# Kernel optimization log

Hardware: AMD Instinct MI355X
Metric: run time of the kernel (lower is better)

The kernel has to match this reference:

```python
import jax, jax.numpy as jnp
import numpy as np

NUM_HEADS = 8
KERNEL = 7
LOW_RANK = 4


def setup_inputs() -> dict:
    key = jax.random.key(0)
    ks = jax.random.split(key, 10)
    B, H, W, C = 4, 56, 56, 256
    nh, K, lr = NUM_HEADS, KERNEL, LOW_RANK
    s = 0.02
    return {
        "x": jax.random.normal(ks[0], (B, H, W, C), jnp.float32),
        "Wq": jax.random.normal(ks[1], (C, nh * lr), jnp.float32) * s,
        "bq": jnp.zeros((nh * lr,), jnp.float32),
        "Wk": jax.random.normal(ks[2], (C, nh * lr), jnp.float32) * s,
        "bk": jnp.zeros((nh * lr,), jnp.float32),
        "Wv": jax.random.normal(ks[3], (C, C), jnp.float32) * s,
        "bv": jnp.zeros((C,), jnp.float32),
        "rpb": jax.random.normal(ks[4], (nh, 2 * K - 1, 2 * K - 1), jnp.float32) * s,
        "Wp": jax.random.normal(ks[5], (C, C), jnp.float32) * s,
        "bp": jnp.zeros((C,), jnp.float32),
    }


def reference(x, Wq, bq, Wk, bk, Wv, bv, rpb, Wp, bp):
    B, H, W, C = x.shape
    nh, K, lr = NUM_HEADS, KERNEL, LOW_RANK
    hd = C // nh
    r = K // 2
    scale = hd ** -0.5

    # Projections. Note: the original uses a raw reshape (B,H,W,nh*lr)->(B,nh,H,W,lr),
    # which we replicate exactly (row-major reshape, no permute).
    q = (x @ Wq + bq).reshape(B, nh, H, W, lr) * scale
    k = (x @ Wk + bk).reshape(B, nh, H, W, lr)
    v = (x @ Wv + bv).reshape(B, nh, H, W, hd)

    # NATTEN window start indices (clamped so each query sees exactly K keys per axis).
    start_h = jnp.clip(jnp.arange(H) - r, 0, H - K)  # (H,)
    start_w = jnp.clip(jnp.arange(W) - r, 0, W - K)  # (W,)
    idx_h = start_h[:, None] + jnp.arange(K)[None, :]  # (H, K)
    idx_w = start_w[:, None] + jnp.arange(K)[None, :]  # (W, K)

    # Gather local K/V windows: (B, nh, H, K, W, K, d)
    k_win = k[:, :, idx_h][:, :, :, :, idx_w]
    v_win = v[:, :, idx_h][:, :, :, :, idx_w]

    # Scores: (B, nh, H, W, K, K)
    attn = jnp.einsum('bhijc,bhikjlc->bhijkl', q, k_win)

    # Relative position bias indices: (key_pos - query_pos) + (K-1)
    bi = idx_h - jnp.arange(H)[:, None] + (K - 1)  # (H, K)
    bj = idx_w - jnp.arange(W)[:, None] + (K - 1)  # (W, K)
    bias = rpb[:, bi][:, :, :, bj]                 # (nh, H, K, W, K)
    attn = attn + bias.transpose(0, 1, 3, 2, 4)[None]  # (B, nh, H, W, K, K)

    attn = jax.nn.softmax(attn.reshape(B, nh, H, W, K * K), axis=-1)
    attn = attn.reshape(B, nh, H, W, K, K)

    # Weighted aggregation of V windows: (B, nh, H, W, hd)
    out = jnp.einsum('bhijkl,bhikjld->bhijd', attn, v_win)
    out = out.transpose(0, 2, 3, 1, 4).reshape(B, H, W, C)
    return out @ Wp + bp
```

## Files before the change

### kernel.cpp

```cpp
#include <hip/hip_runtime.h>
#include <hip/hip_bf16.h>

#define BD 4
#define HD_ 56
#define WD 56
#define CD 256
#define NH 8
#define KW 7
#define LR 4
#define HDIM 32
#define MB (HD_*WD)
#define NROWS (BD*MB)
#define QK_PER_B (HD_*WD*32)
#define V_PER_B  (HD_*WD*256)

typedef short short8 __attribute__((ext_vector_type(8)));
typedef float floatx4 __attribute__((ext_vector_type(4)));

static __device__ inline ushort f2bf(float f) {
    __hip_bfloat16 h = __float2bfloat16(f);
    return *(ushort*)&h;
}
static __device__ inline float bf2f(uint h16) {
    union { uint u; float f; } c; c.u = h16 << 16; return c.f;
}
static __device__ inline float bf2f_hi(uint u) {
    union { uint v; float f; } c; c.v = u & 0xffff0000u; return c.f;
}

__global__ __launch_bounds__(256) void prep_w(
    const float* __restrict__ Wq, const float* __restrict__ Wk,
    const float* __restrict__ Wv, const float* __restrict__ bq,
    const float* __restrict__ bk, const float* __restrict__ bv,
    const float* __restrict__ Wp,
    ushort* __restrict__ WpkT, ushort* __restrict__ WpT, float* __restrict__ pb)
{
    int idx = blockIdx.x * 256 + threadIdx.x;
    if (idx < 81920) {
        int n = idx >> 8, k = idx & 255;
        float v;
        if (n < 32)       v = Wq[k * 32 + n];
        else if (n < 64)  v = Wk[k * 32 + (n - 32)];
        else              v = Wv[k * 256 + (n - 64)];
        WpkT[idx] = f2bf(v);
    } else if (idx < 81920 + 65536) {
        int j = idx - 81920;
        int n = j >> 8, k = j & 255;
        WpT[j] = f2bf(Wp[k * 256 + n]);
    } else if (idx < 81920 + 65536 + 320) {
        int n = idx - (81920 + 65536);
        pb[n] = (n < 32) ? bq[n] : (n < 64) ? bk[n - 32] : bv[n - 64];
    }
}

__global__ __launch_bounds__(256) void mfma_qkv(
    const float* __restrict__ X, const ushort* __restrict__ Bt,
    const float* __restrict__ pb, ushort* __restrict__ Qb,
    ushort* __restrict__ Kb, ushort* __restrict__ Vb)
{
    __shared__ ushort As[128 * 40];
    __shared__ ushort Bs[64 * 40];

    const int t = threadIdx.x;
    const int m0 = blockIdx.y * 128;
    const int n0 = blockIdx.x * 64;
    const int ar = t >> 1;
    const int ac = (t & 1) << 4;
    const int br = t >> 2;
    const int bc = (t & 3) << 3;
    const int lane = t & 63, w = t >> 6;
    const int col = lane & 15, quad = lane >> 4;
    const int q8 = quad << 3;

    floatx4 acc[2][4] = {};

    for (int k0 = 0; k0 < 256; k0 += 32) {
        float4 a0 = *(const float4*)&X[(m0 + ar) * 256 + k0 + ac];
        float4 a1 = *(const float4*)&X[(m0 + ar) * 256 + k0 + ac + 4];
        float4 a2 = *(const float4*)&X[(m0 + ar) * 256 + k0 + ac + 8];
        float4 a3 = *(const float4*)&X[(m0 + ar) * 256 + k0 + ac + 12];
        uint4 bv = *(const uint4*)&Bt[(n0 + br) * 256 + k0 + bc];
        union { ushort h[8]; uint4 u; } p0, p1;
        p0.h[0] = f2bf(a0.x); p0.h[1] = f2bf(a0.y); p0.h[2] = f2bf(a0.z); p0.h[3] = f2bf(a0.w);
        p0.h[4] = f2bf(a1.x); p0.h[5] = f2bf(a1.y); p0.h[6] = f2bf(a1.z); p0.h[7] = f2bf(a1.w);
        p1.h[0] = f2bf(a2.x); p1.h[1] = f2bf(a2.y); p1.h[2] = f2bf(a2.z); p1.h[3] = f2bf(a2.w);
        p1.h[4] = f2bf(a3.x); p1.h[5] = f2bf(a3.y); p1.h[6] = f2bf(a3.z); p1.h[7] = f2bf(a3.w);
        __syncthreads();
        *(uint4*)&As[ar * 40 + ac]     = p0.u;
        *(uint4*)&As[ar * 40 + ac + 8] = p1.u;
        *(uint4*)&Bs[br * 40 + bc]     = bv;
        __syncthreads();
#pragma unroll
        for (int s = 0; s < 2; ++s) {
            short8 af = *(short8*)&As[((w << 5) + (s << 4) + col) * 40 + q8];
#pragma unroll
            for (int nt = 0; nt < 4; ++nt) {
                short8 bf = *(short8*)&Bs[((nt << 4) + col) * 40 + q8];
                acc[s][nt] = __builtin_amdgcn_mfma_f32_16x16x32_bf16(af, bf, acc[s][nt], 0, 0, 0);
            }
        }
    }

#pragma unroll
    for (int s = 0; s < 2; ++s) {
#pragma unroll
        for (int nt = 0; nt < 4; ++nt) {
            int gn = n0 + (nt << 4) + col;
            float bias = pb[gn];
#pragma unroll
            for (int rg = 0; rg < 4; ++rg) {
                int m = m0 + (w << 5) + (s << 4) + (quad << 2) + rg;
                ushort h = f2bf(acc[s][nt][rg] + bias);
                if (n0 == 0 && nt < 2)      Qb[m * 32 + gn] = h;
                else if (n0 == 0)           Kb[m * 32 + (gn - 32)] = h;
                else                        Vb[m * 256 + (gn - 64)] = h;
            }
        }
    }
}

__global__ __launch_bounds__(256) void mfma_out(
    const ushort* __restrict__ Ag, const ushort* __restrict__ Bt,
    const float* __restrict__ bp, float* __restrict__ out)
{
    __shared__ ushort As[128 * 40];
    __shared__ ushort Bs[64 * 40];

    const int t = threadIdx.x;
    const int m0 = blockIdx.y * 128;
    const int n0 = blockIdx.x * 64;
    const int ar = t >> 1;
    const int ac = (t & 1) << 4;
    const int br = t >> 2;
    const int bc = (t & 3) << 3;
    const int lane = t & 63, w = t >> 6;
    const int col = lane & 15, quad = lane >> 4;
    const int q8 = quad << 3;

    floatx4 acc[2][4] = {};

    for (int k0 = 0; k0 < 256; k0 += 32) {
        uint4 av0 = *(const uint4*)&Ag[(m0 + ar) * 256 + k0 + ac];
        uint4 av1 = *(const uint4*)&Ag[(m0 + ar) * 256 + k0 + ac + 8];
        uint4 bv  = *(const uint4*)&Bt[(n0 + br) * 256 + k0 + bc];
        __syncthreads();
        *(uint4*)&As[ar * 40 + ac]     = av0;
        *(uint4*)&As[ar * 40 + ac + 8] = av1;
        *(uint4*)&Bs[br * 40 + bc]     = bv;
        __syncthreads();
#pragma unroll
        for (int s = 0; s < 2; ++s) {
            short8 af = *(short8*)&As[((w << 5) + (s << 4) + col) * 40 + q8];
#pragma unroll
            for (int nt = 0; nt < 4; ++nt) {
                short8 bf = *(short8*)&Bs[((nt << 4) + col) * 40 + q8];
                acc[s][nt] = __builtin_amdgcn_mfma_f32_16x16x32_bf16(af, bf, acc[s][nt], 0, 0, 0);
            }
        }
    }

#pragma unroll
    for (int s = 0; s < 2; ++s) {
#pragma unroll
        for (int nt = 0; nt < 4; ++nt) {
            int gn = n0 + (nt << 4) + col;
            float bias = bp[gn];
#pragma unroll
            for (int rg = 0; rg < 4; ++rg) {
                int m = m0 + (w << 5) + (s << 4) + (quad << 2) + rg;
                out[m * 256 + gn] = acc[s][nt][rg] + bias;
            }
        }
    }
}

__global__ __launch_bounds__(256, 8) void natten_attn_t(
    const ushort* __restrict__ Qb, const ushort* __restrict__ Kb,
    const ushort* __restrict__ Vb, const float* __restrict__ rpb,
    ushort* __restrict__ Ab)
{
    __shared__ float4 Ksf[196];
    __shared__ float4 Vsf[8 * 197];
    __shared__ float  Rs[169];

    const int tj = blockIdx.x, ti = blockIdx.y;
    const int n = blockIdx.z & 7, b = blockIdx.z >> 3;
    const int t = threadIdx.x;
    const int i0 = ti * 8, j0 = tj * 8;
    const int rs = min(max(i0 - 3, 0), HD_ - 14);
    const int cs = min(max(j0 - 3, 0), WD - 14);

    const ushort* kb = Kb + b * QK_PER_B + n * (HD_ * WD * LR);
    const ushort* vb = Vb + b * V_PER_B + n * (HD_ * WD * HDIM);

    if (t < 196) {
        int r = t / 14, c = t % 14;
        union { uint2 u; uint w[2]; } kr;
        kr.u = *(const uint2*)&kb[(rs + r) * (WD * LR) + (cs + c) * LR];
        Ksf[t] = make_float4(bf2f(kr.w[0] & 0xffff), bf2f_hi(kr.w[0]),
                             bf2f(kr.w[1] & 0xffff), bf2f_hi(kr.w[1]));
    }
    if (t < 169) Rs[t] = rpb[n * 169 + t];
    for (int idx = t; idx < 784; idx += 256) {
        int oct = idx & 3, pos = idx >> 2;
        int r = pos / 14, c = pos % 14;
        union { uint4 u; uint w[4]; } vr;
        vr.u = *(const uint4*)&vb[(rs + r) * (WD * HDIM) + (cs + c) * HDIM + oct * 8];
        Vsf[(2 * oct) * 197 + pos] =
            make_float4(bf2f(vr.w[0] & 0xffff), bf2f_hi(vr.w[0]),
                        bf2f(vr.w[1] & 0xffff), bf2f_hi(vr.w[1]));
        Vsf[(2 * oct + 1) * 197 + pos] =
            make_float4(bf2f(vr.w[2] & 0xffff), bf2f_hi(vr.w[2]),
                        bf2f(vr.w[3] & 0xffff), bf2f_hi(vr.w[3]));
    }
    __syncthreads();

    const int q  = t >> 2, p = t & 3;
    const int qi = q >> 3, qj = q & 7;
    const int i = i0 + qi, j = j0 + qj;
    const int sh = min(max(i - 3, 0), HD_ - KW);
    const int sw = min(max(j - 3, 0), WD - KW);
    const int oh = sh - rs, ow = sw - cs;

    union { uint2 u; uint w[2]; } qr;
    qr.u = *(const uint2*)&Qb[b * QK_PER_B + n * (HD_ * WD * LR) + i * (WD * LR) + j * LR];
    const float scale = 0.17677669529663687f;
    float qx = bf2f(qr.w[0] & 0xffff) * scale, qy = bf2f_hi(qr.w[0]) * scale;
    float qz = bf2f(qr.w[1] & 0xffff) * scale, qw = bf2f_hi(qr.w[1]) * scale;

    const int rb0 = (sh - i + 6) * 13 + (sw - j + 6);

    float sum = 0.f;
    float a[8] = {0.f, 0.f, 0.f, 0.f, 0.f, 0.f, 0.f, 0.f};
    const float4* v0 = &Vsf[(2 * p) * 197];
    const float4* v1 = &Vsf[(2 * p + 1) * 197];
    for (int kh = 0; kh < KW; ++kh) {
        int kpos  = (oh + kh) * 14 + ow;
        int rbase = rb0 + kh * 13;
#pragma unroll
        for (int kw = 0; kw < KW; ++kw) {
            float4 kf = Ksf[kpos + kw];
            float d = Rs[rbase + kw];
            d = fmaf(qx, kf.x, d);
            d = fmaf(qy, kf.y, d);
            d = fmaf(qz, kf.z, d);
            d = fmaf(qw, kf.w, d);
            float e = __expf(d);
            sum += e;
            float4 x0 = v0[kpos + kw];
            float4 x1 = v1[kpos + kw];
            a[0] = fmaf(e, x0.x, a[0]); a[1] = fmaf(e, x0.y, a[1]);
            a[2] = fmaf(e, x0.z, a[2]); a[3] = fmaf(e, x0.w, a[3]);
            a[4] = fmaf(e, x1.x, a[4]); a[5] = fmaf(e, x1.y, a[5]);
            a[6] = fmaf(e, x1.z, a[6]); a[7] = fmaf(e, x1.w, a[7]);
        }
    }
    float inv = 1.0f / sum;

    union { ushort h[8]; uint4 u; } pk;
#pragma unroll
    for (int c = 0; c < 8; ++c) pk.h[c] = f2bf(a[c] * inv);
    *(uint4*)&Ab[(((b * HD_ + i) * WD + j)) * CD + n * HDIM + p * 8] = pk.u;
}

extern "C" void kernel_launch(void* const* d_in, const int* in_sizes, int n_in,
                              void* d_out, int out_size, void* d_ws, size_t ws_size,
                              hipStream_t stream) {
    const float* x   = (const float*)d_in[0];
    const float* Wq  = (const float*)d_in[1];
    const float* bq  = (const float*)d_in[2];
    const float* Wk  = (const float*)d_in[3];
    const float* bk  = (const float*)d_in[4];
    const float* Wv  = (const float*)d_in[5];
    const float* bv  = (const float*)d_in[6];
    const float* rpb = (const float*)d_in[7];
    const float* Wp  = (const float*)d_in[8];
    const float* bp  = (const float*)d_in[9];
    float* out = (float*)d_out;

    ushort* WpkT = (ushort*)d_ws;
    ushort* WpT  = WpkT + 81920;
    ushort* Ab   = WpT + 65536;
    ushort* Qb   = Ab + 3211264;
    ushort* Kb   = Qb + BD * QK_PER_B;
    ushort* Vb   = Kb + BD * QK_PER_B;
    float*  pb   = (float*)(Vb + BD * V_PER_B);

    prep_w<<<(81920 + 65536 + 320 + 255) / 256, 256, 0, stream>>>(
        Wq, Wk, Wv, bq, bk, bv, Wp, WpkT, WpT, pb);

    mfma_qkv<<<dim3(5, NROWS / 128), 256, 0, stream>>>(x, WpkT, pb, Qb, Kb, Vb);

    natten_attn_t<<<dim3(7, 7, 32), 256, 0, stream>>>(Qb, Kb, Vb, rpb, Ab);

    mfma_out<<<dim3(4, NROWS / 128), 256, 0, stream>>>(Ab, WpT, bp, out);
}
```

Before: 120.4 us.

## Fuse all four stages into one persistent kernel with grid barriers

Replaces the four separate launches (weight prep, QKV GEMM, neighborhood attention, output GEMM) with one persistent kernel of 512 blocks. Each stage loops over its former blocks as jobs, and software grid barriers built on atomics in the workspace separate the stages. The aim is to remove per-launch overhead and the gaps between kernels. In exchange, the grid barriers rely on all 512 blocks being resident at once, occupancy drops to 2 blocks per CU, and the attention stage (1568 jobs) now runs in several waves with no overlap between stages.

```diff
diff --git a/kernel.cpp b/kernel.cpp
--- a/kernel.cpp
+++ b/kernel.cpp
@@ -14,6 +14,9 @@
 #define QK_PER_B (HD_*WD*32)
 #define V_PER_B  (HD_*WD*256)
 
+#define GRID_G 512
+#define MAGICF 0xC0FFEE01u
+
 typedef short short8 __attribute__((ext_vector_type(8)));
 typedef float floatx4 __attribute__((ext_vector_type(4)));
 
@@ -28,239 +31,274 @@
     union { uint v; float f; } c; c.v = u & 0xffff0000u; return c.f;
 }
 
-__global__ __launch_bounds__(256) void prep_w(
+static __device__ inline void grid_barrier(uint* cnt, uint* gen) {
+    __syncthreads();
+    if (threadIdx.x == 0) {
+        __threadfence();
+        uint g = __hip_atomic_load(gen, __ATOMIC_RELAXED, __HIP_MEMORY_SCOPE_AGENT);
+        uint a = __hip_atomic_fetch_add(cnt, 1u, __ATOMIC_ACQ_REL, __HIP_MEMORY_SCOPE_AGENT);
+        if (a == GRID_G - 1) {
+            __hip_atomic_store(cnt, 0u, __ATOMIC_RELAXED, __HIP_MEMORY_SCOPE_AGENT);
+            __hip_atomic_fetch_add(gen, 1u, __ATOMIC_RELEASE, __HIP_MEMORY_SCOPE_AGENT);
+        } else {
+            while (__hip_atomic_load(gen, __ATOMIC_ACQUIRE, __HIP_MEMORY_SCOPE_AGENT) == g)
+                __builtin_amdgcn_s_sleep(1);
+        }
+        __threadfence();
+    }
+    __syncthreads();
+}
+
+__global__ __launch_bounds__(256, 2) void fused_all(
+    const float* __restrict__ X,
     const float* __restrict__ Wq, const float* __restrict__ Wk,
     const float* __restrict__ Wv, const float* __restrict__ bq,
     const float* __restrict__ bk, const float* __restrict__ bv,
-    const float* __restrict__ Wp,
-    ushort* __restrict__ WpkT, ushort* __restrict__ WpT, float* __restrict__ pb)
+    const float* __restrict__ rpb,
+    const float* __restrict__ Wp, const float* __restrict__ bp,
+    ushort* __restrict__ WpkT, ushort* __restrict__ WpT,
+    float* __restrict__ pb,
+    ushort* __restrict__ Qb, ushort* __restrict__ Kb, ushort* __restrict__ Vb,
+    ushort* __restrict__ Ab, float* __restrict__ out,
+    uint* __restrict__ bar)
 {
-    int idx = blockIdx.x * 256 + threadIdx.x;
-    if (idx < 81920) {
-        int n = idx >> 8, k = idx & 255;
-        float v;
-        if (n < 32)       v = Wq[k * 32 + n];
-        else if (n < 64)  v = Wk[k * 32 + (n - 32)];
-        else              v = Wv[k * 256 + (n - 64)];
-        WpkT[idx] = f2bf(v);
-    } else if (idx < 81920 + 65536) {
-        int j = idx - 81920;
-        int n = j >> 8, k = j & 255;
-        WpT[j] = f2bf(Wp[k * 256 + n]);
-    } else if (idx < 81920 + 65536 + 320) {
-        int n = idx - (81920 + 65536);
-        pb[n] = (n < 32) ? bq[n] : (n < 64) ? bk[n - 32] : bv[n - 64];
-    }
-}
-
-__global__ __launch_bounds__(256) void mfma_qkv(
-    const float* __restrict__ X, const ushort* __restrict__ Bt,
-    const float* __restrict__ pb, ushort* __restrict__ Qb,
-    ushort* __restrict__ Kb, ushort* __restrict__ Vb)
-{
-    __shared__ ushort As[128 * 40];
-    __shared__ ushort Bs[64 * 40];
+    __shared__ __align__(16) char smem[29184];
 
     const int t = threadIdx.x;
-    const int m0 = blockIdx.y * 128;
-    const int n0 = blockIdx.x * 64;
-    const int ar = t >> 1;
-    const int ac = (t & 1) << 4;
-    const int br = t >> 2;
-    const int bc = (t & 3) << 3;
-    const int lane = t & 63, w = t >> 6;
-    const int col = lane & 15, quad = lane >> 4;
-    const int q8 = quad << 3;
-
-    floatx4 acc[2][4] = {};
-
-    for (int k0 = 0; k0 < 256; k0 += 32) {
-        float4 a0 = *(const float4*)&X[(m0 + ar) * 256 + k0 + ac];
-        float4 a1 = *(const float4*)&X[(m0 + ar) * 256 + k0 + ac + 4];
-        float4 a2 = *(const float4*)&X[(m0 + ar) * 256 + k0 + ac + 8];
-        float4 a3 = *(const float4*)&X[(m0 + ar) * 256 + k0 + ac + 12];
-        uint4 bv = *(const uint4*)&Bt[(n0 + br) * 256 + k0 + bc];
-        union { ushort h[8]; uint4 u; } p0, p1;
-        p0.h[0] = f2bf(a0.x); p0.h[1] = f2bf(a0.y); p0.h[2] = f2bf(a0.z); p0.h[3] = f2bf(a0.w);
-        p0.h[4] = f2bf(a1.x); p0.h[5] = f2bf(a1.y); p0.h[6] = f2bf(a1.z); p0.h[7] = f2bf(a1.w);
-        p1.h[0] = f2bf(a2.x); p1.h[1] = f2bf(a2.y); p1.h[2] = f2bf(a2.z); p1.h[3] = f2bf(a2.w);
-        p1.h[4] = f2bf(a3.x); p1.h[5] = f2bf(a3.y); p1.h[6] = f2bf(a3.z); p1.h[7] = f2bf(a3.w);
-        __syncthreads();
-        *(uint4*)&As[ar * 40 + ac]     = p0.u;
-        *(uint4*)&As[ar * 40 + ac + 8] = p1.u;
-        *(uint4*)&Bs[br * 40 + bc]     = bv;
-        __syncthreads();
-#pragma unroll
-        for (int s = 0; s < 2; ++s) {
-            short8 af = *(short8*)&As[((w << 5) + (s << 4) + col) * 40 + q8];
-#pragma unroll
-            for (int nt = 0; nt < 4; ++nt) {
-                short8 bf = *(short8*)&Bs[((nt << 4) + col) * 40 + q8];
-                acc[s][nt] = __builtin_amdgcn_mfma_f32_16x16x32_bf16(af, bf, acc[s][nt], 0, 0, 0);
-            }
-        }
-    }
-
-#pragma unroll
-    for (int s = 0; s < 2; ++s) {
-#pragma unroll
-        for (int nt = 0; nt < 4; ++nt) {
-            int gn = n0 + (nt << 4) + col;
-            float bias = pb[gn];
-#pragma unroll
-            for (int rg = 0; rg < 4; ++rg) {
-                int m = m0 + (w << 5) + (s << 4) + (quad << 2) + rg;
-                ushort h = f2bf(acc[s][nt][rg] + bias);
-                if (n0 == 0 && nt < 2)      Qb[m * 32 + gn] = h;
-                else if (n0 == 0)           Kb[m * 32 + (gn - 32)] = h;
-                else                        Vb[m * 256 + (gn - 64)] = h;
-            }
-        }
-    }
-}
-
-__global__ __launch_bounds__(256) void mfma_out(
-    const ushort* __restrict__ Ag, const ushort* __restrict__ Bt,
-    const float* __restrict__ bp, float* __restrict__ out)
-{
-    __shared__ ushort As[128 * 40];
-    __shared__ ushort Bs[64 * 40];
-
-    const int t = threadIdx.x;
-    const int m0 = blockIdx.y * 128;
-    const int n0 = blockIdx.x * 64;
-    const int ar = t >> 1;
-    const int ac = (t & 1) << 4;
-    const int br = t >> 2;
-    const int bc = (t & 3) << 3;
-    const int lane = t & 63, w = t >> 6;
-    const int col = lane & 15, quad = lane >> 4;
-    const int q8 = quad << 3;
-
-    floatx4 acc[2][4] = {};
-
-    for (int k0 = 0; k0 < 256; k0 += 32) {
-        uint4 av0 = *(const uint4*)&Ag[(m0 + ar) * 256 + k0 + ac];
-        uint4 av1 = *(const uint4*)&Ag[(m0 + ar) * 256 + k0 + ac + 8];
-        uint4 bv  = *(const uint4*)&Bt[(n0 + br) * 256 + k0 + bc];
-        __syncthreads();
-        *(uint4*)&As[ar * 40 + ac]     = av0;
-        *(uint4*)&As[ar * 40 + ac + 8] = av1;
-        *(uint4*)&Bs[br * 40 + bc]     = bv;
-        __syncthreads();
-#pragma unroll
-        for (int s = 0; s < 2; ++s) {
-            short8 af = *(short8*)&As[((w << 5) + (s << 4) + col) * 40 + q8];
-#pragma unroll
-            for (int nt = 0; nt < 4; ++nt) {
-                short8 bf = *(short8*)&Bs[((nt << 4) + col) * 40 + q8];
-                acc[s][nt] = __builtin_amdgcn_mfma_f32_16x16x32_bf16(af, bf, acc[s][nt], 0, 0, 0);
-            }
-        }
-    }
-
-#pragma unroll
-    for (int s = 0; s < 2; ++s) {
-#pragma unroll
-        for (int nt = 0; nt < 4; ++nt) {
-            int gn = n0 + (nt << 4) + col;
-            float bias = bp[gn];
-#pragma unroll
-            for (int rg = 0; rg < 4; ++rg) {
-                int m = m0 + (w << 5) + (s << 4) + (quad << 2) + rg;
-                out[m * 256 + gn] = acc[s][nt][rg] + bias;
-            }
-        }
-    }
-}
-
-__global__ __launch_bounds__(256, 8) void natten_attn_t(
-    const ushort* __restrict__ Qb, const ushort* __restrict__ Kb,
-    const ushort* __restrict__ Vb, const float* __restrict__ rpb,
-    ushort* __restrict__ Ab)
-{
-    __shared__ float4 Ksf[196];
-    __shared__ float4 Vsf[8 * 197];
-    __shared__ float  Rs[169];
-
-    const int tj = blockIdx.x, ti = blockIdx.y;
-    const int n = blockIdx.z & 7, b = blockIdx.z >> 3;
-    const int t = threadIdx.x;
-    const int i0 = ti * 8, j0 = tj * 8;
-    const int rs = min(max(i0 - 3, 0), HD_ - 14);
-    const int cs = min(max(j0 - 3, 0), WD - 14);
-
-    const ushort* kb = Kb + b * QK_PER_B + n * (HD_ * WD * LR);
-    const ushort* vb = Vb + b * V_PER_B + n * (HD_ * WD * HDIM);
-
-    if (t < 196) {
-        int r = t / 14, c = t % 14;
-        union { uint2 u; uint w[2]; } kr;
-        kr.u = *(const uint2*)&kb[(rs + r) * (WD * LR) + (cs + c) * LR];
-        Ksf[t] = make_float4(bf2f(kr.w[0] & 0xffff), bf2f_hi(kr.w[0]),
-                             bf2f(kr.w[1] & 0xffff), bf2f_hi(kr.w[1]));
-    }
-    if (t < 169) Rs[t] = rpb[n * 169 + t];
-    for (int idx = t; idx < 784; idx += 256) {
-        int oct = idx & 3, pos = idx >> 2;
-        int r = pos / 14, c = pos % 14;
-        union { uint4 u; uint w[4]; } vr;
-        vr.u = *(const uint4*)&vb[(rs + r) * (WD * HDIM) + (cs + c) * HDIM + oct * 8];
-        Vsf[(2 * oct) * 197 + pos] =
-            make_float4(bf2f(vr.w[0] & 0xffff), bf2f_hi(vr.w[0]),
-                        bf2f(vr.w[1] & 0xffff), bf2f_hi(vr.w[1]));
-        Vsf[(2 * oct + 1) * 197 + pos] =
-            make_float4(bf2f(vr.w[2] & 0xffff), bf2f_hi(vr.w[2]),
-                        bf2f(vr.w[3] & 0xffff), bf2f_hi(vr.w[3]));
+    const int blk = blockIdx.x;
+    uint* flag = bar + 0;
+    uint* cnt  = bar + 1;
+    uint* gen  = bar + 2;
+
+    if (blk == 0) {
+        if (t == 0) {
+            if (__hip_atomic_load(flag, __ATOMIC_ACQUIRE, __HIP_MEMORY_SCOPE_AGENT) != MAGICF) {
+                __hip_atomic_store(cnt, 0u, __ATOMIC_RELAXED, __HIP_MEMORY_SCOPE_AGENT);
+                __hip_atomic_store(gen, 0u, __ATOMIC_RELAXED, __HIP_MEMORY_SCOPE_AGENT);
+                __hip_atomic_store(flag, MAGICF, __ATOMIC_RELEASE, __HIP_MEMORY_SCOPE_AGENT);
+            }
+        }
+    } else if (t == 0) {
+        while (__hip_atomic_load(flag, __ATOMIC_ACQUIRE, __HIP_MEMORY_SCOPE_AGENT) != MAGICF)
+            __builtin_amdgcn_s_sleep(1);
     }
     __syncthreads();
 
-    const int q  = t >> 2, p = t & 3;
-    const int qi = q >> 3, qj = q & 7;
-    const int i = i0 + qi, j = j0 + qj;
-    const int sh = min(max(i - 3, 0), HD_ - KW);
-    const int sw = min(max(j - 3, 0), WD - KW);
-    const int oh = sh - rs, ow = sw - cs;
-
-    union { uint2 u; uint w[2]; } qr;
-    qr.u = *(const uint2*)&Qb[b * QK_PER_B + n * (HD_ * WD * LR) + i * (WD * LR) + j * LR];
-    const float scale = 0.17677669529663687f;
-    float qx = bf2f(qr.w[0] & 0xffff) * scale, qy = bf2f_hi(qr.w[0]) * scale;
-    float qz = bf2f(qr.w[1] & 0xffff) * scale, qw = bf2f_hi(qr.w[1]) * scale;
-
-    const int rb0 = (sh - i + 6) * 13 + (sw - j + 6);
-
-    float sum = 0.f;
-    float a[8] = {0.f, 0.f, 0.f, 0.f, 0.f, 0.f, 0.f, 0.f};
-    const float4* v0 = &Vsf[(2 * p) * 197];
-    const float4* v1 = &Vsf[(2 * p + 1) * 197];
-    for (int kh = 0; kh < KW; ++kh) {
-        int kpos  = (oh + kh) * 14 + ow;
-        int rbase = rb0 + kh * 13;
-#pragma unroll
-        for (int kw = 0; kw < KW; ++kw) {
-            float4 kf = Ksf[kpos + kw];
-            float d = Rs[rbase + kw];
-            d = fmaf(qx, kf.x, d);
-            d = fmaf(qy, kf.y, d);
-            d = fmaf(qz, kf.z, d);
-            d = fmaf(qw, kf.w, d);
-            float e = __expf(d);
-            sum += e;
-            float4 x0 = v0[kpos + kw];
-            float4 x1 = v1[kpos + kw];
-            a[0] = fmaf(e, x0.x, a[0]); a[1] = fmaf(e, x0.y, a[1]);
-            a[2] = fmaf(e, x0.z, a[2]); a[3] = fmaf(e, x0.w, a[3]);
-            a[4] = fmaf(e, x1.x, a[4]); a[5] = fmaf(e, x1.y, a[5]);
-            a[6] = fmaf(e, x1.z, a[6]); a[7] = fmaf(e, x1.w, a[7]);
-        }
-    }
-    float inv = 1.0f / sum;
-
-    union { ushort h[8]; uint4 u; } pk;
-#pragma unroll
-    for (int c = 0; c < 8; ++c) pk.h[c] = f2bf(a[c] * inv);
-    *(uint4*)&Ab[(((b * HD_ + i) * WD + j)) * CD + n * HDIM + p * 8] = pk.u;
+    for (int idx = blk * 256 + t; idx < 81920 + 65536 + 320; idx += GRID_G * 256) {
+        if (idx < 81920) {
+            int n = idx >> 8, k = idx & 255;
+            float v;
+            if (n < 32)       v = Wq[k * 32 + n];
+            else if (n < 64)  v = Wk[k * 32 + (n - 32)];
+            else              v = Wv[k * 256 + (n - 64)];
+            WpkT[idx] = f2bf(v);
+        } else if (idx < 81920 + 65536) {
+            int jj = idx - 81920;
+            int n = jj >> 8, k = jj & 255;
+            WpT[jj] = f2bf(Wp[k * 256 + n]);
+        } else {
+            int n = idx - (81920 + 65536);
+            pb[n] = (n < 32) ? bq[n] : (n < 64) ? bk[n - 32] : bv[n - 64];
+        }
+    }
+    grid_barrier(cnt, gen);
+
+    {
+        ushort* As = (ushort*)smem;
+        ushort* Bs = As + 128 * 40;
+        const int ar = t >> 1, ac = (t & 1) << 4;
+        const int br = t >> 2, bc = (t & 3) << 3;
+        const int lane = t & 63, w = t >> 6;
+        const int col = lane & 15, quad = lane >> 4;
+        const int q8 = quad << 3;
+
+        for (int job = blk; job < 5 * 98; job += GRID_G) {
+            const int n0 = (job % 5) * 64;
+            const int m0 = (job / 5) * 128;
+            floatx4 acc[2][4] = {};
+            for (int k0 = 0; k0 < 256; k0 += 32) {
+                float4 a0 = *(const float4*)&X[(m0 + ar) * 256 + k0 + ac];
+                float4 a1 = *(const float4*)&X[(m0 + ar) * 256 + k0 + ac + 4];
+                float4 a2 = *(const float4*)&X[(m0 + ar) * 256 + k0 + ac + 8];
+                float4 a3 = *(const float4*)&X[(m0 + ar) * 256 + k0 + ac + 12];
+                uint4 bv2 = *(const uint4*)&WpkT[(n0 + br) * 256 + k0 + bc];
+                union { ushort h[8]; uint4 u; } p0, p1;
+                p0.h[0] = f2bf(a0.x); p0.h[1] = f2bf(a0.y); p0.h[2] = f2bf(a0.z); p0.h[3] = f2bf(a0.w);
+                p0.h[4] = f2bf(a1.x); p0.h[5] = f2bf(a1.y); p0.h[6] = f2bf(a1.z); p0.h[7] = f2bf(a1.w);
+                p1.h[0] = f2bf(a2.x); p1.h[1] = f2bf(a2.y); p1.h[2] = f2bf(a2.z); p1.h[3] = f2bf(a2.w);
+                p1.h[4] = f2bf(a3.x); p1.h[5] = f2bf(a3.y); p1.h[6] = f2bf(a3.z); p1.h[7] = f2bf(a3.w);
+                __syncthreads();
+                *(uint4*)&As[ar * 40 + ac]     = p0.u;
+                *(uint4*)&As[ar * 40 + ac + 8] = p1.u;
+                *(uint4*)&Bs[br * 40 + bc]     = bv2;
+                __syncthreads();
+#pragma unroll
+                for (int s = 0; s < 2; ++s) {
+                    short8 af = *(short8*)&As[((w << 5) + (s << 4) + col) * 40 + q8];
+#pragma unroll
+                    for (int nt = 0; nt < 4; ++nt) {
+                        short8 bf = *(short8*)&Bs[((nt << 4) + col) * 40 + q8];
+                        acc[s][nt] = __builtin_amdgcn_mfma_f32_16x16x32_bf16(af, bf, acc[s][nt], 0, 0, 0);
+                    }
+                }
+            }
+#pragma unroll
+            for (int s = 0; s < 2; ++s) {
+#pragma unroll
+                for (int nt = 0; nt < 4; ++nt) {
+                    int gn = n0 + (nt << 4) + col;
+                    float bias = pb[gn];
+#pragma unroll
+                    for (int rg = 0; rg < 4; ++rg) {
+                        int m = m0 + (w << 5) + (s << 4) + (quad << 2) + rg;
+                        ushort h = f2bf(acc[s][nt][rg] + bias);
+                        if (n0 == 0 && nt < 2)      Qb[m * 32 + gn] = h;
+                        else if (n0 == 0)           Kb[m * 32 + (gn - 32)] = h;
+                        else                        Vb[m * 256 + (gn - 64)] = h;
+                    }
+                }
+            }
+            __syncthreads();
+        }
+    }
+    grid_barrier(cnt, gen);
+
+    {
+        float4* Ksf = (float4*)smem;
+        float4* Vsf = Ksf + 196;
+        float*  Rs  = (float*)(Vsf + 8 * 197);
+
+        for (int job = blk; job < 7 * 7 * 32; job += GRID_G) {
+            const int tj = job % 7, ti = (job / 7) % 7, z = job / 49;
+            const int n = z & 7, b = z >> 3;
+            const int i0 = ti * 8, j0 = tj * 8;
+            const int rs = min(max(i0 - 3, 0), HD_ - 14);
+            const int cs = min(max(j0 - 3, 0), WD - 14);
+
+            const ushort* kb = Kb + b * QK_PER_B + n * (HD_ * WD * LR);
+            const ushort* vb = Vb + b * V_PER_B + n * (HD_ * WD * HDIM);
+
+            if (t < 196) {
+                int r = t / 14, c = t % 14;
+                union { uint2 u; uint w[2]; } kr;
+                kr.u = *(const uint2*)&kb[(rs + r) * (WD * LR) + (cs + c) * LR];
+                Ksf[t] = make_float4(bf2f(kr.w[0] & 0xffff), bf2f_hi(kr.w[0]),
+                                     bf2f(kr.w[1] & 0xffff), bf2f_hi(kr.w[1]));
+            }
+            if (t < 169) Rs[t] = rpb[n * 169 + t];
+            for (int idx = t; idx < 784; idx += 256) {
+                int oct = idx & 3, pos = idx >> 2;
+                int r = pos / 14, c = pos % 14;
+                union { uint4 u; uint w[4]; } vr;
+                vr.u = *(const uint4*)&vb[(rs + r) * (WD * HDIM) + (cs + c) * HDIM + oct * 8];
+                Vsf[(2 * oct) * 197 + pos] =
+                    make_float4(bf2f(vr.w[0] & 0xffff), bf2f_hi(vr.w[0]),
+                                bf2f(vr.w[1] & 0xffff), bf2f_hi(vr.w[1]));
+                Vsf[(2 * oct + 1) * 197 + pos] =
+                    make_float4(bf2f(vr.w[2] & 0xffff), bf2f_hi(vr.w[2]),
+                                bf2f(vr.w[3] & 0xffff), bf2f_hi(vr.w[3]));
+            }
+            __syncthreads();
+
+            const int q  = t >> 2, p = t & 3;
+            const int qi = q >> 3, qj = q & 7;
+            const int i = i0 + qi, j = j0 + qj;
+            const int sh = min(max(i - 3, 0), HD_ - KW);
+            const int sw = min(max(j - 3, 0), WD - KW);
+            const int oh = sh - rs, ow = sw - cs;
+
+            union { uint2 u; uint w[2]; } qr;
+            qr.u = *(const uint2*)&Qb[b * QK_PER_B + n * (HD_ * WD * LR) + i * (WD * LR) + j * LR];
+            const float scale = 0.17677669529663687f;
+            float qx = bf2f(qr.w[0] & 0xffff) * scale, qy = bf2f_hi(qr.w[0]) * scale;
+            float qz = bf2f(qr.w[1] & 0xffff) * scale, qw = bf2f_hi(qr.w[1]) * scale;
+
+            const int rb0 = (sh - i + 6) * 13 + (sw - j + 6);
+
+            float sum = 0.f;
+            float a[8] = {0.f, 0.f, 0.f, 0.f, 0.f, 0.f, 0.f, 0.f};
+            const float4* v0 = &Vsf[(2 * p) * 197];
+            const float4* v1 = &Vsf[(2 * p + 1) * 197];
+            for (int kh = 0; kh < KW; ++kh) {
+                int kpos  = (oh + kh) * 14 + ow;
+                int rbase = rb0 + kh * 13;
+#pragma unroll
+                for (int kw = 0; kw < KW; ++kw) {
+                    float4 kf = Ksf[kpos + kw];
+                    float d = Rs[rbase + kw];
+                    d = fmaf(qx, kf.x, d);
+                    d = fmaf(qy, kf.y, d);
+                    d = fmaf(qz, kf.z, d);
+                    d = fmaf(qw, kf.w, d);
+                    float e = __expf(d);
+                    sum += e;
+                    float4 x0 = v0[kpos + kw];
+                    float4 x1 = v1[kpos + kw];
+                    a[0] = fmaf(e, x0.x, a[0]); a[1] = fmaf(e, x0.y, a[1]);
+                    a[2] = fmaf(e, x0.z, a[2]); a[3] = fmaf(e, x0.w, a[3]);
+                    a[4] = fmaf(e, x1.x, a[4]); a[5] = fmaf(e, x1.y, a[5]);
+                    a[6] = fmaf(e, x1.z, a[6]); a[7] = fmaf(e, x1.w, a[7]);
+                }
+            }
+            float inv = 1.0f / sum;
+
+            union { ushort h[8]; uint4 u; } pk;
+#pragma unroll
+            for (int c = 0; c < 8; ++c) pk.h[c] = f2bf(a[c] * inv);
+            *(uint4*)&Ab[(((b * HD_ + i) * WD + j)) * CD + n * HDIM + p * 8] = pk.u;
+            __syncthreads();
+        }
+    }
+    grid_barrier(cnt, gen);
+
+    {
+        ushort* As = (ushort*)smem;
+        ushort* Bs = As + 128 * 40;
+        const int ar = t >> 1, ac = (t & 1) << 4;
+        const int br = t >> 2, bc = (t & 3) << 3;
+        const int lane = t & 63, w = t >> 6;
+        const int col = lane & 15, quad = lane >> 4;
+        const int q8 = quad << 3;
+
+        for (int job = blk; job < 4 * 98; job += GRID_G) {
+            const int n0 = (job % 4) * 64;
+            const int m0 = (job / 4) * 128;
+            floatx4 acc[2][4] = {};
+            for (int k0 = 0; k0 < 256; k0 += 32) {
+                uint4 av0 = *(const uint4*)&Ab[(m0 + ar) * 256 + k0 + ac];
+                uint4 av1 = *(const uint4*)&Ab[(m0 + ar) * 256 + k0 + ac + 8];
+                uint4 bv2 = *(const uint4*)&WpT[(n0 + br) * 256 + k0 + bc];
+                __syncthreads();
+                *(uint4*)&As[ar * 40 + ac]     = av0;
+                *(uint4*)&As[ar * 40 + ac + 8] = av1;
+                *(uint4*)&Bs[br * 40 + bc]     = bv2;
+                __syncthreads();
+#pragma unroll
+                for (int s = 0; s < 2; ++s) {
+                    short8 af = *(short8*)&As[((w << 5) + (s << 4) + col) * 40 + q8];
+#pragma unroll
+                    for (int nt = 0; nt < 4; ++nt) {
+                        short8 bf = *(short8*)&Bs[((nt << 4) + col) * 40 + q8];
+                        acc[s][nt] = __builtin_amdgcn_mfma_f32_16x16x32_bf16(af, bf, acc[s][nt], 0, 0, 0);
+                    }
+                }
+            }
+#pragma unroll
+            for (int s = 0; s < 2; ++s) {
+#pragma unroll
+                for (int nt = 0; nt < 4; ++nt) {
+                    int gn = n0 + (nt << 4) + col;
+                    float bias = bp[gn];
+#pragma unroll
+                    for (int rg = 0; rg < 4; ++rg) {
+                        int m = m0 + (w << 5) + (s << 4) + (quad << 2) + rg;
+                        out[m * 256 + gn] = acc[s][nt][rg] + bias;
+                    }
+                }
+            }
+            __syncthreads();
+        }
+    }
 }
 
 extern "C" void kernel_launch(void* const* d_in, const int* in_sizes, int n_in,
@@ -285,13 +323,9 @@
     ushort* Kb   = Qb + BD * QK_PER_B;
     ushort* Vb   = Kb + BD * QK_PER_B;
     float*  pb   = (float*)(Vb + BD * V_PER_B);
-
-    prep_w<<<(81920 + 65536 + 320 + 255) / 256, 256, 0, stream>>>(
-        Wq, Wk, Wv, bq, bk, bv, Wp, WpkT, WpT, pb);
-
-    mfma_qkv<<<dim3(5, NROWS / 128), 256, 0, stream>>>(x, WpkT, pb, Qb, Kb, Vb);
-
-    natten_attn_t<<<dim3(7, 7, 32), 256, 0, stream>>>(Qb, Kb, Vb, rpb, Ab);
-
-    mfma_out<<<dim3(4, NROWS / 128), 256, 0, stream>>>(Ab, WpT, bp, out);
-}
+    uint*   bar  = (uint*)(pb + 320);
+
+    fused_all<<<GRID_G, 256, 0, stream>>>(
+        x, Wq, Wk, Wv, bq, bk, bv, rpb, Wp, bp,
+        WpkT, WpT, pb, Qb, Kb, Vb, Ab, out, bar);
+}
```

Measured after the change: 400.9 us. 3.33x slower.

## Fuse weight transpose and bf16 conversion into GEMM kernels, drop prep kernel

Applied to the files above, without the earlier changes.

Removes the separate prep_w launch that transposed and converted the weights to bf16 in workspace. Each GEMM block now loads its full 64x256 weight slice from the fp32 weights, converts it and stores it transposed into a padded shared buffer once, then reads B fragments from it across all k-steps. This saves a kernel launch and the per-k-step global B loads. In exchange, every block redoes the weight conversion, uses more LDS (about 34 KB), and issues scalar strided shared-memory stores that may cause bank conflicts.

```diff
diff --git a/kernel.cpp b/kernel.cpp
--- a/kernel.cpp
+++ b/kernel.cpp
@@ -14,6 +14,8 @@
 #define QK_PER_B (HD_*WD*32)
 #define V_PER_B  (HD_*WD*256)
 
+#define BSTR 264
+
 typedef short short8 __attribute__((ext_vector_type(8)));
 typedef float floatx4 __attribute__((ext_vector_type(4)));
 
@@ -28,46 +30,38 @@
     union { uint v; float f; } c; c.v = u & 0xffff0000u; return c.f;
 }
 
-__global__ __launch_bounds__(256) void prep_w(
+__global__ __launch_bounds__(256) void mfma_qkv(
+    const float* __restrict__ X,
     const float* __restrict__ Wq, const float* __restrict__ Wk,
     const float* __restrict__ Wv, const float* __restrict__ bq,
     const float* __restrict__ bk, const float* __restrict__ bv,
-    const float* __restrict__ Wp,
-    ushort* __restrict__ WpkT, ushort* __restrict__ WpT, float* __restrict__ pb)
+    ushort* __restrict__ Qb, ushort* __restrict__ Kb, ushort* __restrict__ Vb)
 {
-    int idx = blockIdx.x * 256 + threadIdx.x;
-    if (idx < 81920) {
-        int n = idx >> 8, k = idx & 255;
-        float v;
-        if (n < 32)       v = Wq[k * 32 + n];
-        else if (n < 64)  v = Wk[k * 32 + (n - 32)];
-        else              v = Wv[k * 256 + (n - 64)];
-        WpkT[idx] = f2bf(v);
-    } else if (idx < 81920 + 65536) {
-        int j = idx - 81920;
-        int n = j >> 8, k = j & 255;
-        WpT[j] = f2bf(Wp[k * 256 + n]);
-    } else if (idx < 81920 + 65536 + 320) {
-        int n = idx - (81920 + 65536);
-        pb[n] = (n < 32) ? bq[n] : (n < 64) ? bk[n - 32] : bv[n - 64];
-    }
-}
-
-__global__ __launch_bounds__(256) void mfma_qkv(
-    const float* __restrict__ X, const ushort* __restrict__ Bt,
-    const float* __restrict__ pb, ushort* __restrict__ Qb,
-    ushort* __restrict__ Kb, ushort* __restrict__ Vb)
-{
+    __shared__ ushort Bs[64 * BSTR];
     __shared__ ushort As[128 * 40];
-    __shared__ ushort Bs[64 * 40];
 
     const int t = threadIdx.x;
     const int m0 = blockIdx.y * 128;
     const int n0 = blockIdx.x * 64;
-    const int ar = t >> 1;
-    const int ac = (t & 1) << 4;
-    const int br = t >> 2;
-    const int bc = (t & 3) << 3;
+
+    {
+        const int kr = t >> 4;
+        const int cg = (t & 15) << 2;
+        const int gn = n0 + cg;
+        for (int it = 0; it < 16; ++it) {
+            int k = (it << 4) + kr;
+            float4 wv;
+            if (gn < 32)      wv = *(const float4*)&Wq[k * 32 + gn];
+            else if (gn < 64) wv = *(const float4*)&Wk[k * 32 + (gn - 32)];
+            else              wv = *(const float4*)&Wv[k * 256 + (gn - 64)];
+            Bs[(cg + 0) * BSTR + k] = f2bf(wv.x);
+            Bs[(cg + 1) * BSTR + k] = f2bf(wv.y);
+            Bs[(cg + 2) * BSTR + k] = f2bf(wv.z);
+            Bs[(cg + 3) * BSTR + k] = f2bf(wv.w);
+        }
+    }
+
+    const int ar = t >> 1, ac = (t & 1) << 4;
     const int lane = t & 63, w = t >> 6;
     const int col = lane & 15, quad = lane >> 4;
     const int q8 = quad << 3;
@@ -79,7 +73,6 @@
         float4 a1 = *(const float4*)&X[(m0 + ar) * 256 + k0 + ac + 4];
         float4 a2 = *(const float4*)&X[(m0 + ar) * 256 + k0 + ac + 8];
         float4 a3 = *(const float4*)&X[(m0 + ar) * 256 + k0 + ac + 12];
-        uint4 bv = *(const uint4*)&Bt[(n0 + br) * 256 + k0 + bc];
         union { ushort h[8]; uint4 u; } p0, p1;
         p0.h[0] = f2bf(a0.x); p0.h[1] = f2bf(a0.y); p0.h[2] = f2bf(a0.z); p0.h[3] = f2bf(a0.w);
         p0.h[4] = f2bf(a1.x); p0.h[5] = f2bf(a1.y); p0.h[6] = f2bf(a1.z); p0.h[7] = f2bf(a1.w);
@@ -88,14 +81,13 @@
         __syncthreads();
         *(uint4*)&As[ar * 40 + ac]     = p0.u;
         *(uint4*)&As[ar * 40 + ac + 8] = p1.u;
-        *(uint4*)&Bs[br * 40 + bc]     = bv;
         __syncthreads();
 #pragma unroll
         for (int s = 0; s < 2; ++s) {
             short8 af = *(short8*)&As[((w << 5) + (s << 4) + col) * 40 + q8];
 #pragma unroll
             for (int nt = 0; nt < 4; ++nt) {
-                short8 bf = *(short8*)&Bs[((nt << 4) + col) * 40 + q8];
+                short8 bf = *(short8*)&Bs[((nt << 4) + col) * BSTR + k0 + q8];
                 acc[s][nt] = __builtin_amdgcn_mfma_f32_16x16x32_bf16(af, bf, acc[s][nt], 0, 0, 0);
             }
         }
@@ -106,7 +98,7 @@
 #pragma unroll
         for (int nt = 0; nt < 4; ++nt) {
             int gn = n0 + (nt << 4) + col;
-            float bias = pb[gn];
+            float bias = (gn < 32) ? bq[gn] : (gn < 64) ? bk[gn - 32] : bv[gn - 64];
 #pragma unroll
             for (int rg = 0; rg < 4; ++rg) {
                 int m = m0 + (w << 5) + (s << 4) + (quad << 2) + rg;
@@ -120,19 +112,31 @@
 }
 
 __global__ __launch_bounds__(256) void mfma_out(
-    const ushort* __restrict__ Ag, const ushort* __restrict__ Bt,
+    const ushort* __restrict__ Ag, const float* __restrict__ Wp,
     const float* __restrict__ bp, float* __restrict__ out)
 {
+    __shared__ ushort Bs[64 * BSTR];
     __shared__ ushort As[128 * 40];
-    __shared__ ushort Bs[64 * 40];
 
     const int t = threadIdx.x;
     const int m0 = blockIdx.y * 128;
     const int n0 = blockIdx.x * 64;
-    const int ar = t >> 1;
-    const int ac = (t & 1) << 4;
-    const int br = t >> 2;
-    const int bc = (t & 3) << 3;
+
+    {
+        const int kr = t >> 4;
+        const int cg = (t & 15) << 2;
+        const int gn = n0 + cg;
+        for (int it = 0; it < 16; ++it) {
+            int k = (it << 4) + kr;
+            float4 wv = *(const float4*)&Wp[k * 256 + gn];
+            Bs[(cg + 0) * BSTR + k] = f2bf(wv.x);
+            Bs[(cg + 1) * BSTR + k] = f2bf(wv.y);
+            Bs[(cg + 2) * BSTR + k] = f2bf(wv.z);
+            Bs[(cg + 3) * BSTR + k] = f2bf(wv.w);
+        }
+    }
+
+    const int ar = t >> 1, ac = (t & 1) << 4;
     const int lane = t & 63, w = t >> 6;
     const int col = lane & 15, quad = lane >> 4;
     const int q8 = quad << 3;
@@ -142,18 +146,16 @@
     for (int k0 = 0; k0 < 256; k0 += 32) {
         uint4 av0 = *(const uint4*)&Ag[(m0 + ar) * 256 + k0 + ac];
         uint4 av1 = *(const uint4*)&Ag[(m0 + ar) * 256 + k0 + ac + 8];
-        uint4 bv  = *(const uint4*)&Bt[(n0 + br) * 256 + k0 + bc];
         __syncthreads();
         *(uint4*)&As[ar * 40 + ac]     = av0;
         *(uint4*)&As[ar * 40 + ac + 8] = av1;
-        *(uint4*)&Bs[br * 40 + bc]     = bv;
         __syncthreads();
 #pragma unroll
         for (int s = 0; s < 2; ++s) {
             short8 af = *(short8*)&As[((w << 5) + (s << 4) + col) * 40 + q8];
 #pragma unroll
             for (int nt = 0; nt < 4; ++nt) {
-                short8 bf = *(short8*)&Bs[((nt << 4) + col) * 40 + q8];
+                short8 bf = *(short8*)&Bs[((nt << 4) + col) * BSTR + k0 + q8];
                 acc[s][nt] = __builtin_amdgcn_mfma_f32_16x16x32_bf16(af, bf, acc[s][nt], 0, 0, 0);
             }
         }
@@ -278,20 +280,15 @@
     const float* bp  = (const float*)d_in[9];
     float* out = (float*)d_out;
 
-    ushort* WpkT = (ushort*)d_ws;
-    ushort* WpT  = WpkT + 81920;
-    ushort* Ab   = WpT + 65536;
-    ushort* Qb   = Ab + 3211264;
-    ushort* Kb   = Qb + BD * QK_PER_B;
-    ushort* Vb   = Kb + BD * QK_PER_B;
-    float*  pb   = (float*)(Vb + BD * V_PER_B);
-
-    prep_w<<<(81920 + 65536 + 320 + 255) / 256, 256, 0, stream>>>(
-        Wq, Wk, Wv, bq, bk, bv, Wp, WpkT, WpT, pb);
-
-    mfma_qkv<<<dim3(5, NROWS / 128), 256, 0, stream>>>(x, WpkT, pb, Qb, Kb, Vb);
+    ushort* Ab = (ushort*)d_ws;
+    ushort* Qb = Ab + 3211264;
+    ushort* Kb = Qb + BD * QK_PER_B;
+    ushort* Vb = Kb + BD * QK_PER_B;
+
+    mfma_qkv<<<dim3(5, NROWS / 128), 256, 0, stream>>>(
+        x, Wq, Wk, Wv, bq, bk, bv, Qb, Kb, Vb);
 
     natten_attn_t<<<dim3(7, 7, 32), 256, 0, stream>>>(Qb, Kb, Vb, rpb, Ab);
 
-    mfma_out<<<dim3(4, NROWS / 128), 256, 0, stream>>>(Ab, WpT, bp, out);
-}
+    mfma_out<<<dim3(4, NROWS / 128), 256, 0, stream>>>(Ab, Wp, bp, out);
+}
```

Measured after the change: 125.0 us. +3.8%, slower.
